# Kernel optimization log

Hardware: AMD Instinct MI355X
Metric: run time of the kernel (lower is better)

## Reference

```python
import jax, jax.numpy as jnp
import numpy as np

MAX_MARGIN = -25.0
MIN_MARGIN = 50.0
LAMDA = 1.0
INV_LAMDA = 1.0


def setup_inputs() -> dict:
    key = jax.random.key(0)
    k1, k2 = jax.random.split(key)
    n, c = 8192, 10000
    inputs = jax.random.normal(k1, (n, c), dtype=jnp.float32)
    targets = jax.random.randint(k2, (n,), 0, c, dtype=jnp.int64)
    return {"inputs": inputs, "targets": targets}


def reference(inputs, targets):
    n, c = inputs.shape
    # one-hot of target positions, built via comparison (no scatter loop)
    is_tgt = jnp.arange(c, dtype=targets.dtype)[None, :] == targets[:, None]  # [n, c] bool
    mask = jnp.where(is_tgt, -LAMDA, INV_LAMDA)          # sign/weight mask
    margin = jnp.where(is_tgt, MIN_MARGIN, MAX_MARGIN)   # per-entry margin
    loss_m = jnp.maximum(mask * (inputs - margin), 0.0)  # hinge clamp
    loss_inter = jnp.where(is_tgt, 0.0, loss_m)          # zero-out target column
    inv_n = jnp.float32(1.0) / n
    return (loss_m.sum() * inv_n, loss_inter.sum() * inv_n)
```

## Files before the change

kernel.cpp:

```cpp
#include <hip/hip_runtime.h>

#define N_ROWS 8192LL
#define N_COLS 10000LL
#define GRID_BLKS 2048


__global__ void __launch_bounds__(256) hinge_partials(const float4* __restrict__ in4,
                                                      const float* __restrict__ in,
                                                      const int* __restrict__ tgt,
                                                      float2* __restrict__ ws) {
    const long long n4 = N_ROWS * N_COLS / 4;
    const long long stride = (long long)GRID_BLKS * 256;
    const long long gid = (long long)blockIdx.x * blockDim.x + threadIdx.x;

    float acc = 0.0f;
    for (long long i = gid; i < n4; i += stride) {
        float4 v = in4[i];
        acc += fmaxf(v.x + 25.0f, 0.0f) + fmaxf(v.y + 25.0f, 0.0f)
             + fmaxf(v.z + 25.0f, 0.0f) + fmaxf(v.w + 25.0f, 0.0f);
    }

    float d0 = acc, d1 = acc;
    if (gid < N_ROWS) {
        int t = tgt[gid];
        float x = in[gid * N_COLS + (long long)t];
        float plus  = fmaxf(x + 25.0f, 0.0f);
        float hinge = fmaxf(50.0f - x, 0.0f);
        d0 += hinge - plus;
        d1 -= plus;
    }

    #pragma unroll
    for (int off = 32; off > 0; off >>= 1) {
        d0 += __shfl_down(d0, off, 64);
        d1 += __shfl_down(d1, off, 64);
    }
    __shared__ float s0[4], s1[4];
    const int lane = threadIdx.x & 63;
    const int wid  = threadIdx.x >> 6;
    if (lane == 0) { s0[wid] = d0; s1[wid] = d1; }
    __syncthreads();
    if (threadIdx.x == 0) {
        ws[blockIdx.x] = make_float2(s0[0] + s0[1] + s0[2] + s0[3],
                                     s1[0] + s1[1] + s1[2] + s1[3]);
    }
}

__global__ void __launch_bounds__(1024) hinge_reduce(const float2* __restrict__ ws,
                                                     float* __restrict__ out) {
    float2 a = ws[threadIdx.x];
    float2 b = ws[threadIdx.x + 1024];
    float d0 = a.x + b.x;
    float d1 = a.y + b.y;
    #pragma unroll
    for (int off = 32; off > 0; off >>= 1) {
        d0 += __shfl_down(d0, off, 64);
        d1 += __shfl_down(d1, off, 64);
    }
    __shared__ float s0[16], s1[16];
    const int lane = threadIdx.x & 63;
    const int wid  = threadIdx.x >> 6;
    if (lane == 0) { s0[wid] = d0; s1[wid] = d1; }
    __syncthreads();
    if (threadIdx.x == 0) {
        float t0 = 0.0f, t1 = 0.0f;
        #pragma unroll
        for (int k = 0; k < 16; ++k) { t0 += s0[k]; t1 += s1[k]; }
        const float inv_n = 1.0f / (float)N_ROWS;
        out[0] = t0 * inv_n;
        out[1] = t1 * inv_n;
    }
}

extern "C" void kernel_launch(void* const* d_in, const int* in_sizes, int n_in,
                              void* d_out, int out_size, void* d_ws, size_t ws_size,
                              hipStream_t stream) {
    const float* inputs = (const float*)d_in[0];
    const int* targets = (const int*)d_in[1];
    float* out = (float*)d_out;
    float2* ws = (float2*)d_ws;

    hinge_partials<<<GRID_BLKS, 256, 0, stream>>>((const float4*)inputs, inputs, targets, ws);
    hinge_reduce<<<1, 1024, 0, stream>>>(ws, out);
}
```

Measured before the change: 56.43 us.

## Fuse final reduction into main kernel via last-block atomic counter

```diff
diff --git a/kernel.cpp b/kernel.cpp
--- a/kernel.cpp
+++ b/kernel.cpp
@@ -3,19 +3,26 @@
 #define N_ROWS 8192LL
 #define N_COLS 10000LL
 #define GRID_BLKS 2048
+#define BLOCK 256
 
 
-__global__ void __launch_bounds__(256) hinge_partials(const float4* __restrict__ in4,
-                                                      const float* __restrict__ in,
-                                                      const int* __restrict__ tgt,
-                                                      float2* __restrict__ ws) {
+typedef float f4 __attribute__((ext_vector_type(4)));
+
+union F2U { float2 f; unsigned long long u; };
+
+__global__ void __launch_bounds__(BLOCK) hinge_onepass(const f4* __restrict__ in4,
+                                                       const float* __restrict__ in,
+                                                       const int* __restrict__ tgt,
+                                                       float2* __restrict__ ws,
+                                                       unsigned* __restrict__ counter,
+                                                       float* __restrict__ out) {
     const long long n4 = N_ROWS * N_COLS / 4;
-    const long long stride = (long long)GRID_BLKS * 256;
-    const long long gid = (long long)blockIdx.x * blockDim.x + threadIdx.x;
+    const long long stride = (long long)GRID_BLKS * BLOCK;
+    const long long gid = (long long)blockIdx.x * BLOCK + threadIdx.x;
 
     float acc = 0.0f;
     for (long long i = gid; i < n4; i += stride) {
-        float4 v = in4[i];
+        f4 v = __builtin_nontemporal_load(&in4[i]);
         acc += fmaxf(v.x + 25.0f, 0.0f) + fmaxf(v.y + 25.0f, 0.0f)
              + fmaxf(v.z + 25.0f, 0.0f) + fmaxf(v.w + 25.0f, 0.0f);
     }
@@ -36,39 +43,44 @@
         d1 += __shfl_down(d1, off, 64);
     }
     __shared__ float s0[4], s1[4];
+    __shared__ bool amLast;
     const int lane = threadIdx.x & 63;
     const int wid  = threadIdx.x >> 6;
     if (lane == 0) { s0[wid] = d0; s1[wid] = d1; }
     __syncthreads();
+
     if (threadIdx.x == 0) {
-        ws[blockIdx.x] = make_float2(s0[0] + s0[1] + s0[2] + s0[3],
-                                     s1[0] + s1[1] + s1[2] + s1[3]);
+        F2U p;
+        p.f = make_float2(s0[0] + s0[1] + s0[2] + s0[3],
+                          s1[0] + s1[1] + s1[2] + s1[3]);
+        __hip_atomic_store((unsigned long long*)&ws[blockIdx.x], p.u,
+                           __ATOMIC_RELEASE, __HIP_MEMORY_SCOPE_AGENT);
+        unsigned prev = __hip_atomic_fetch_add(counter, 1u,
+                           __ATOMIC_ACQ_REL, __HIP_MEMORY_SCOPE_AGENT);
+        amLast = (prev == GRID_BLKS - 1);
     }
-}
+    __syncthreads();
 
-__global__ void __launch_bounds__(1024) hinge_reduce(const float2* __restrict__ ws,
-                                                     float* __restrict__ out) {
-    float2 a = ws[threadIdx.x];
-    float2 b = ws[threadIdx.x + 1024];
-    float d0 = a.x + b.x;
-    float d1 = a.y + b.y;
-    #pragma unroll
-    for (int off = 32; off > 0; off >>= 1) {
-        d0 += __shfl_down(d0, off, 64);
-        d1 += __shfl_down(d1, off, 64);
-    }
-    __shared__ float s0[16], s1[16];
-    const int lane = threadIdx.x & 63;
-    const int wid  = threadIdx.x >> 6;
-    if (lane == 0) { s0[wid] = d0; s1[wid] = d1; }
-    __syncthreads();
-    if (threadIdx.x == 0) {
+    if (amLast) {
         float t0 = 0.0f, t1 = 0.0f;
+        for (int k = threadIdx.x; k < GRID_BLKS; k += BLOCK) {
+            F2U p;
+            p.u = __hip_atomic_load((const unsigned long long*)&ws[k],
+                                    __ATOMIC_RELAXED, __HIP_MEMORY_SCOPE_AGENT);
+            t0 += p.f.x; t1 += p.f.y;
+        }
         #pragma unroll
-        for (int k = 0; k < 16; ++k) { t0 += s0[k]; t1 += s1[k]; }
-        const float inv_n = 1.0f / (float)N_ROWS;
-        out[0] = t0 * inv_n;
-        out[1] = t1 * inv_n;
+        for (int off = 32; off > 0; off >>= 1) {
+            t0 += __shfl_down(t0, off, 64);
+            t1 += __shfl_down(t1, off, 64);
+        }
+        if (lane == 0) { s0[wid] = t0; s1[wid] = t1; }
+        __syncthreads();
+        if (threadIdx.x == 0) {
+            const float inv_n = 1.0f / (float)N_ROWS;
+            out[0] = (s0[0] + s0[1] + s0[2] + s0[3]) * inv_n;
+            out[1] = (s1[0] + s1[1] + s1[2] + s1[3]) * inv_n;
+        }
     }
 }
 
@@ -79,7 +91,10 @@
     const int* targets = (const int*)d_in[1];
     float* out = (float*)d_out;
     float2* ws = (float2*)d_ws;
+    unsigned* counter = (unsigned*)((char*)d_ws + GRID_BLKS * sizeof(float2));
 
-    hinge_partials<<<GRID_BLKS, 256, 0, stream>>>((const float4*)inputs, inputs, targets, ws);
-    hinge_reduce<<<1, 1024, 0, stream>>>(ws, out);
+    (void)hipMemsetAsync(counter, 0, sizeof(unsigned), stream);
+
+    hinge_onepass<<<GRID_BLKS, BLOCK, 0, stream>>>((const f4*)inputs, inputs,
+                                                   targets, ws, counter, out);
 }
```

Result: slower. 138.5 us (+145.4%).
